# Performance work log

Hardware: AMD Instinct MI355X
Metric: run time of the kernel (lower is better)

Reference implementation:

```python
import jax, jax.numpy as jnp
import numpy as np

N_HEADS = 16  # matches init_kwargs

def setup_inputs() -> dict:
    key = jax.random.key(0)
    kq, kk, kv = jax.random.split(key, 3)
    B, L, S, D = 4, 2048, 2048, 1024
    queries = jax.random.normal(kq, (B, L, D), dtype=jnp.float32)
    keys = jax.random.normal(kk, (B, S, D), dtype=jnp.float32)
    values = jax.random.normal(kv, (B, S, D), dtype=jnp.float32)
    # TriangularCausalMask: True above the diagonal (positions to mask)
    causal = jnp.triu(jnp.ones((L, S), dtype=bool), k=1)
    attn_mask = jnp.broadcast_to(causal[None, None], (B, 1, L, S))
    return {"queries": queries, "keys": keys, "values": values, "attn_mask": attn_mask}

def reference(queries, keys, values, attn_mask):
    B, L, _ = queries.shape
    S = keys.shape[1]
    H = N_HEADS
    q = queries.reshape(B, L, H, -1)   # (B,L,H,E)
    k = keys.reshape(B, S, H, -1)      # (B,S,H,E)
    v = values.reshape(B, S, H, -1)    # (B,S,H,E)
    scale = 1.0 / jnp.sqrt(jnp.asarray(q.shape[-1], dtype=q.dtype))
    scores = jnp.einsum('blhe,bshe->bhls', q, k)          # (B,H,L,S)
    scores = jnp.where(attn_mask, -jnp.inf, scores)        # masked_fill_
    A = jax.nn.softmax(scale * scores, axis=-1)            # dropout is identity (p=0 / eval)
    V = jnp.einsum('bhls,bshd->blhd', A, v)                # (B,L,H,E)
    return V.reshape(B, L, -1)
```

## Files before the change

kernel.cpp:

```cpp
#include <hip/hip_runtime.h>
#include <hip/hip_bf16.h>

typedef __attribute__((ext_vector_type(8))) short short8;
typedef __attribute__((ext_vector_type(4))) short short4v;
typedef __attribute__((ext_vector_type(4))) float floatx4;

constexpr int B = 4, L = 2048, H = 16, E = 64, D = 1024;
constexpr int STR = 72;
constexpr float SCL_LOG2E = 0.125f * 1.4426950408889634f;

__device__ __forceinline__ short bf16_bits(float x) {
    __hip_bfloat16 b = __float2bfloat16(x);
    return *(const short*)&b;
}

__device__ __forceinline__ short8 packq8(float4 a, float4 c, float scl) {
    short8 r;
    r[0] = bf16_bits(a.x * scl); r[1] = bf16_bits(a.y * scl);
    r[2] = bf16_bits(a.z * scl); r[3] = bf16_bits(a.w * scl);
    r[4] = bf16_bits(c.x * scl); r[5] = bf16_bits(c.y * scl);
    r[6] = bf16_bits(c.z * scl); r[7] = bf16_bits(c.w * scl);
    return r;
}

__device__ __forceinline__ void load_lds16(const short* g, short* l) {
    __builtin_amdgcn_global_load_lds(
        (const __attribute__((address_space(1))) unsigned int*)g,
        (__attribute__((address_space(3))) unsigned int*)l, 16, 0, 0);
}

__global__ __launch_bounds__(256)
void prep_kv(const float* __restrict__ K, const float* __restrict__ V,
             short* __restrict__ Kb, short* __restrict__ Vt)
{
    __shared__ __align__(16) short vt[64 * STR];
    const int tid = threadIdx.x;
    const int bh = blockIdx.x >> 5, kt = blockIdx.x & 31;
    const int b = bh >> 4, h = bh & 15;

    const float* Kp = K + ((size_t)(b * L + kt * 64)) * D + h * E;
    const float* Vp = V + ((size_t)(b * L + kt * 64)) * D + h * E;
    short* Kop = Kb + ((size_t)(bh * 32 + kt)) * 4096;
    short* Vop = Vt + ((size_t)(bh * 32 + kt)) * 4096;

    #pragma unroll
    for (int it = 0; it < 2; ++it) {
        int f = it * 256 + tid;
        int nt = f >> 7, hh = (f >> 6) & 1, qd = (f >> 4) & 3, cc = f & 15;
        int s = nt * 16 + cc, d0 = hh * 32 + qd * 8;
        const float* p = Kp + (size_t)s * D + d0;
        float4 x = *(const float4*)p;
        float4 y = *(const float4*)(p + 4);
        union { short sh[8]; uint4 u; } pk;
        pk.sh[0] = bf16_bits(x.x); pk.sh[1] = bf16_bits(x.y);
        pk.sh[2] = bf16_bits(x.z); pk.sh[3] = bf16_bits(x.w);
        pk.sh[4] = bf16_bits(y.x); pk.sh[5] = bf16_bits(y.y);
        pk.sh[6] = bf16_bits(y.z); pk.sh[7] = bf16_bits(y.w);
        *(uint4*)(Kop + (size_t)f * 8) = pk.u;
    }

    #pragma unroll
    for (int p = 0; p < 4; ++p) {
        int idx = p * 256 + tid;
        int s = idx >> 4, c4 = (idx & 15) * 4;
        float4 g = *(const float4*)(Vp + (size_t)s * D + c4);
        vt[(c4 + 0) * STR + s] = bf16_bits(g.x);
        vt[(c4 + 1) * STR + s] = bf16_bits(g.y);
        vt[(c4 + 2) * STR + s] = bf16_bits(g.z);
        vt[(c4 + 3) * STR + s] = bf16_bits(g.w);
    }
    __syncthreads();

    #pragma unroll
    for (int it = 0; it < 2; ++it) {
        int f16 = it * 256 + tid;
        int f8 = f16 * 2;
        int st = f8 >> 8, dt = (f8 >> 6) & 3, qd = (f8 >> 4) & 3;
        int cA = f8 & 15;
        int dA = dt * 16 + cA, dB = dA + 1;
        int s0 = st * 16 + qd * 4;
        uint2 a = *(const uint2*)&vt[dA * STR + s0];
        uint2 c = *(const uint2*)&vt[dB * STR + s0];
        uint4 u; u.x = a.x; u.y = a.y; u.z = c.x; u.w = c.y;
        *(uint4*)(Vop + (size_t)f16 * 8) = u;
    }
}

__device__ __forceinline__ void step_single(
    const short* __restrict__ kc, const short* __restrict__ vc,
    short8 qf0, short8 qf1, int mrow, int s_base, int cnt, bool diag,
    floatx4 (&o)[4], float& lsum, int lane)
{
    short4v pa[4];
    #pragma unroll
    for (int nt = 0; nt < 4; ++nt) {
        if (nt < cnt) {
            short8 kb0 = *(const short8*)&kc[nt * 1024 + lane * 8];
            short8 kb1 = *(const short8*)&kc[nt * 1024 + 512 + lane * 8];
            floatx4 acc = (floatx4){0.f, 0.f, 0.f, 0.f};
            acc = __builtin_amdgcn_mfma_f32_16x16x32_bf16(kb0, qf0, acc, 0, 0, 0);
            acc = __builtin_amdgcn_mfma_f32_16x16x32_bf16(kb1, qf1, acc, 0, 0, 0);
            if (diag && nt == cnt - 1) {
                const int s0 = s_base + nt * 16;
                #pragma unroll
                for (int r = 0; r < 4; ++r)
                    if (s0 + r > mrow) acc[r] = -__builtin_inff();
            }
            #pragma unroll
            for (int r = 0; r < 4; ++r) {
                float p = __builtin_amdgcn_exp2f(acc[r]);
                lsum += p;
                pa[nt][r] = bf16_bits(p);
            }
        }
    }
    #pragma unroll
    for (int st = 0; st < 4; ++st) {
        if (st < cnt) {
            #pragma unroll
            for (int dt = 0; dt < 4; ++dt) {
                short4v vb = *(const short4v*)&vc[(st * 4 + dt) * 256 + lane * 4];
                o[dt] = __builtin_amdgcn_mfma_f32_16x16x16bf16_1k(pa[st], vb, o[dt], 0, 0, 0);
            }
        }
    }
}

__device__ __forceinline__ void step_merged(
    const short* __restrict__ kc, const short* __restrict__ vc,
    short8 qfA0, short8 qfA1, short8 qfB0, short8 qfB1,
    int mrowB, int s_base, int cntB, bool diagB,
    floatx4 (&oA)[4], floatx4 (&oB)[4], float& lA, float& lB, int lane)
{
    short4v paA[4], paB[4];
    #pragma unroll
    for (int nt = 0; nt < 4; ++nt) {
        short8 kb0 = *(const short8*)&kc[nt * 1024 + lane * 8];
        short8 kb1 = *(const short8*)&kc[nt * 1024 + 512 + lane * 8];
        floatx4 a = (floatx4){0.f, 0.f, 0.f, 0.f};
        a = __builtin_amdgcn_mfma_f32_16x16x32_bf16(kb0, qfA0, a, 0, 0, 0);
        a = __builtin_amdgcn_mfma_f32_16x16x32_bf16(kb1, qfA1, a, 0, 0, 0);
        #pragma unroll
        for (int r = 0; r < 4; ++r) {
            float p = __builtin_amdgcn_exp2f(a[r]);
            lA += p;
            paA[nt][r] = bf16_bits(p);
        }
        if (nt < cntB) {
            floatx4 bb = (floatx4){0.f, 0.f, 0.f, 0.f};
            bb = __builtin_amdgcn_mfma_f32_16x16x32_bf16(kb0, qfB0, bb, 0, 0, 0);
            bb = __builtin_amdgcn_mfma_f32_16x16x32_bf16(kb1, qfB1, bb, 0, 0, 0);
            if (diagB && nt == cntB - 1) {
                const int s0 = s_base + nt * 16;
                #pragma unroll
                for (int r = 0; r < 4; ++r)
                    if (s0 + r > mrowB) bb[r] = -__builtin_inff();
            }
            #pragma unroll
            for (int r = 0; r < 4; ++r) {
                float p = __builtin_amdgcn_exp2f(bb[r]);
                lB += p;
                paB[nt][r] = bf16_bits(p);
            }
        }
    }
    #pragma unroll
    for (int st = 0; st < 4; ++st) {
        #pragma unroll
        for (int dt = 0; dt < 4; ++dt) {
            short4v vb = *(const short4v*)&vc[(st * 4 + dt) * 256 + lane * 4];
            oA[dt] = __builtin_amdgcn_mfma_f32_16x16x16bf16_1k(paA[st], vb, oA[dt], 0, 0, 0);
            if (st < cntB)
                oB[dt] = __builtin_amdgcn_mfma_f32_16x16x16bf16_1k(paB[st], vb, oB[dt], 0, 0, 0);
        }
    }
}

__device__ __forceinline__ void store_frag(
    float lsum, const floatx4 (&o)[4], float* __restrict__ Op,
    int row_base, int c16, int quad)
{
    lsum += __shfl_xor(lsum, 16);
    lsum += __shfl_xor(lsum, 32);
    const int row0 = row_base + quad * 4;
    #pragma unroll
    for (int r = 0; r < 4; ++r) {
        const float inv = 1.f / __shfl(lsum, quad * 4 + r);
        #pragma unroll
        for (int dt = 0; dt < 4; ++dt)
            Op[(size_t)(row0 + r) * D + dt * 16 + c16] = o[dt][r] * inv;
    }
}

__global__ __launch_bounds__(256, 4)
void attn_fwd_p(const float* __restrict__ Q, const short* __restrict__ Kb,
                const short* __restrict__ Vt, float* __restrict__ O)
{
    __shared__ __align__(16) short k_s[2 * 4096];
    __shared__ __align__(16) short v_s[2 * 4096];

    const int tid  = threadIdx.x;
    const int wave = tid >> 6;
    const int lane = tid & 63;
    const int c16  = lane & 15;
    const int quad = lane >> 4;

    const int i  = (int)blockIdx.x;
    const int bh = ((i >> 7) << 3) | (i & 7);
    const int pp = (i >> 3) & 15;
    const int b  = bh >> 4;
    const int h  = bh & 15;

    const float* Qp  = Q  + ((size_t)b * L) * D + h * E;
    const short* Kbp = Kb + ((size_t)bh * 32) * 4096;
    const short* Vtp = Vt + ((size_t)bh * 32) * 4096;
    float*       Op  = O  + ((size_t)b * L) * D + h * E;

    const int qtA = 31 - pp, qtB = pp;
    const int nA  = qtA + 1;
    const int mA  = qtA * 64 + wave * 16;
    const int mB  = qtB * 64 + wave * 16;

    const float* qra = Qp + (size_t)(mA + c16) * D + quad * 8;
    short8 qfA0 = packq8(*(const float4*)(qra),      *(const float4*)(qra + 4),  SCL_LOG2E);
    short8 qfA1 = packq8(*(const float4*)(qra + 32), *(const float4*)(qra + 36), SCL_LOG2E);
    const float* qrb = Qp + (size_t)(mB + c16) * D + quad * 8;
    short8 qfB0 = packq8(*(const float4*)(qrb),      *(const float4*)(qrb + 4),  SCL_LOG2E);
    short8 qfB1 = packq8(*(const float4*)(qrb + 32), *(const float4*)(qrb + 36), SCL_LOG2E);

    #pragma unroll
    for (int it = 0; it < 2; ++it) {
        int c = it * 256 + tid;
        load_lds16(Kbp + (size_t)c * 8, k_s + c * 8);
        load_lds16(Vtp + (size_t)c * 8, v_s + c * 8);
    }

    floatx4 oA[4], oB[4];
    #pragma unroll
    for (int dt = 0; dt < 4; ++dt) {
        oA[dt] = (floatx4){0.f, 0.f, 0.f, 0.f};
        oB[dt] = (floatx4){0.f, 0.f, 0.f, 0.f};
    }
    float lA = 0.f, lB = 0.f;

    for (int t = 0; t < nA; ++t) {
        __syncthreads();
        const short* kc = k_s + (t & 1) * 4096;
        const short* vc = v_s + (t & 1) * 4096;

        if (t + 1 < nA) {
            const size_t nb = (size_t)(t + 1) * 4096;
            short* kn = k_s + ((t + 1) & 1) * 4096;
            short* vn = v_s + ((t + 1) & 1) * 4096;
            #pragma unroll
            for (int it = 0; it < 2; ++it) {
                int c = it * 256 + tid;
                load_lds16(Kbp + nb + (size_t)c * 8, kn + c * 8);
                load_lds16(Vtp + nb + (size_t)c * 8, vn + c * 8);
            }
        }

        __builtin_amdgcn_s_setprio(1);
        const int sb = t * 64 + quad * 4;
        if (t < qtB) {
            step_merged(kc, vc, qfA0, qfA1, qfB0, qfB1, 0, sb, 4, false,
                        oA, oB, lA, lB, lane);
        } else if (t == qtB) {
            step_merged(kc, vc, qfA0, qfA1, qfB0, qfB1, mB + c16, sb, wave + 1, true,
                        oA, oB, lA, lB, lane);
        } else if (t < qtA) {
            step_single(kc, vc, qfA0, qfA1, 0, sb, 4, false, oA, lA, lane);
        } else {
            step_single(kc, vc, qfA0, qfA1, mA + c16, sb, wave + 1, true, oA, lA, lane);
        }
        __builtin_amdgcn_s_setprio(0);
    }

    store_frag(lA, oA, Op, mA, c16, quad);
    store_frag(lB, oB, Op, mB, c16, quad);
}

__global__ __launch_bounds__(256, 2)
void attn_fwd_fb(const float* __restrict__ Q, const float* __restrict__ K,
                 const float* __restrict__ V, float* __restrict__ O)
{
    constexpr int FSTR = 72;
    constexpr int FQT = 64;
    __shared__ __align__(16) short q_s[FQT * FSTR];
    __shared__ __align__(16) short k_s[64 * FSTR];
    __shared__ __align__(16) short vt_s[E * FSTR];
    __shared__ __align__(16) short p_s[4][16 * FSTR];

    const int tid  = threadIdx.x;
    const int wave = tid >> 6;
    const int lane = tid & 63;
    const int c16  = lane & 15;
    const int quad = lane >> 4;

    const int nqt = L / FQT;
    const int qt  = (nqt - 1) - (int)(blockIdx.x % nqt);
    const int bh  = blockIdx.x / nqt;
    const int b   = bh >> 4;
    const int h   = bh & 15;
    const int q_base = qt * FQT;

    const float* Qp = Q + ((size_t)b * L) * D + h * E;
    const float* Kp = K + ((size_t)b * L) * D + h * E;
    const float* Vp = V + ((size_t)b * L) * D + h * E;
    float*       Op = O + ((size_t)b * L) * D + h * E;

    #pragma unroll
    for (int p = 0; p < 4; ++p) {
        int idx = p * 256 + tid;
        int r = idx >> 4, c4 = (idx & 15) * 4;
        float4 f = *(const float4*)(Qp + (size_t)(q_base + r) * D + c4);
        union { short s[4]; uint2 u; } pk;
        pk.s[0] = bf16_bits(f.x); pk.s[1] = bf16_bits(f.y);
        pk.s[2] = bf16_bits(f.z); pk.s[3] = bf16_bits(f.w);
        *(uint2*)&q_s[r * FSTR + c4] = pk.u;
    }
    __syncthreads();

    short8 qf0 = *(const short8*)&q_s[(wave * 16 + c16) * FSTR + quad * 8];
    short8 qf1 = *(const short8*)&q_s[(wave * 16 + c16) * FSTR + 32 + quad * 8];

    floatx4 o_acc[4];
    #pragma unroll
    for (int nt = 0; nt < 4; ++nt) o_acc[nt] = (floatx4){0.f, 0.f, 0.f, 0.f};
    float m_run[4], l_run[4];
    #pragma unroll
    for (int r = 0; r < 4; ++r) { m_run[r] = -__builtin_inff(); l_run[r] = 0.f; }

    for (int t = 0; t <= qt; ++t) {
        const int k_base = t * 64;
        __syncthreads();
        #pragma unroll
        for (int p = 0; p < 4; ++p) {
            int idx = p * 256 + tid;
            int r = idx >> 4, c4 = (idx & 15) * 4;
            float4 f = *(const float4*)(Kp + (size_t)(k_base + r) * D + c4);
            union { short s[4]; uint2 u; } pk;
            pk.s[0] = bf16_bits(f.x); pk.s[1] = bf16_bits(f.y);
            pk.s[2] = bf16_bits(f.z); pk.s[3] = bf16_bits(f.w);
            *(uint2*)&k_s[r * FSTR + c4] = pk.u;
        }
        #pragma unroll
        for (int p = 0; p < 4; ++p) {
            int s  = lane;
            int dg = p * 4 + wave;
            float4 f = *(const float4*)(Vp + (size_t)(k_base + s) * D + dg * 4);
            vt_s[(dg * 4 + 0) * FSTR + s] = bf16_bits(f.x);
            vt_s[(dg * 4 + 1) * FSTR + s] = bf16_bits(f.y);
            vt_s[(dg * 4 + 2) * FSTR + s] = bf16_bits(f.z);
            vt_s[(dg * 4 + 3) * FSTR + s] = bf16_bits(f.w);
        }
        __syncthreads();

        floatx4 sc[4];
        #pragma unroll
        for (int nt = 0; nt < 4; ++nt) {
            floatx4 acc = (floatx4){0.f, 0.f, 0.f, 0.f};
            short8 b0 = *(const short8*)&k_s[(nt * 16 + c16) * FSTR + quad * 8];
            short8 b1 = *(const short8*)&k_s[(nt * 16 + c16) * FSTR + 32 + quad * 8];
            acc = __builtin_amdgcn_mfma_f32_16x16x32_bf16(qf0, b0, acc, 0, 0, 0);
            acc = __builtin_amdgcn_mfma_f32_16x16x32_bf16(qf1, b1, acc, 0, 0, 0);
            sc[nt] = acc;
        }

        const int q_row0 = q_base + wave * 16 + quad * 4;
        #pragma unroll
        for (int nt = 0; nt < 4; ++nt) {
            const int k_col = k_base + nt * 16 + c16;
            #pragma unroll
            for (int r = 0; r < 4; ++r) {
                float s = sc[nt][r] * SCL_LOG2E;
                sc[nt][r] = (k_col <= q_row0 + r) ? s : -__builtin_inff();
            }
        }

        float alpha[4];
        #pragma unroll
        for (int r = 0; r < 4; ++r) {
            float mx = fmaxf(fmaxf(sc[0][r], sc[1][r]), fmaxf(sc[2][r], sc[3][r]));
            mx = fmaxf(mx, __shfl_xor(mx, 1));
            mx = fmaxf(mx, __shfl_xor(mx, 2));
            mx = fmaxf(mx, __shfl_xor(mx, 4));
            mx = fmaxf(mx, __shfl_xor(mx, 8));
            const float m_new = fmaxf(m_run[r], mx);
            alpha[r] = exp2f(m_run[r] - m_new);
            m_run[r] = m_new;
        }
        float psum[4] = {0.f, 0.f, 0.f, 0.f};
        #pragma unroll
        for (int nt = 0; nt < 4; ++nt) {
            #pragma unroll
            for (int r = 0; r < 4; ++r) {
                float p = exp2f(sc[nt][r] - m_run[r]);
                sc[nt][r] = p;
                psum[r] += p;
            }
        }
        #pragma unroll
        for (int r = 0; r < 4; ++r) {
            float s = psum[r];
            s += __shfl_xor(s, 1);
            s += __shfl_xor(s, 2);
            s += __shfl_xor(s, 4);
            s += __shfl_xor(s, 8);
            l_run[r] = l_run[r] * alpha[r] + s;
            #pragma unroll
            for (int nt = 0; nt < 4; ++nt) o_acc[nt][r] *= alpha[r];
        }

        short* pw = &p_s[wave][0];
        #pragma unroll
        for (int nt = 0; nt < 4; ++nt) {
            #pragma unroll
            for (int r = 0; r < 4; ++r)
                pw[(quad * 4 + r) * FSTR + nt * 16 + c16] = bf16_bits(sc[nt][r]);
        }
        __syncthreads();

        #pragma unroll
        for (int kc = 0; kc < 2; ++kc) {
            short8 pa = *(const short8*)&pw[c16 * FSTR + kc * 32 + quad * 8];
            #pragma unroll
            for (int nt = 0; nt < 4; ++nt) {
                short8 vb = *(const short8*)&vt_s[(nt * 16 + c16) * FSTR + kc * 32 + quad * 8];
                o_acc[nt] = __builtin_amdgcn_mfma_f32_16x16x32_bf16(pa, vb, o_acc[nt], 0, 0, 0);
            }
        }
    }

    const int q_row0 = q_base + wave * 16 + quad * 4;
    #pragma unroll
    for (int r = 0; r < 4; ++r) {
        const float inv_l = 1.f / l_run[r];
        #pragma unroll
        for (int nt = 0; nt < 4; ++nt)
            Op[(size_t)(q_row0 + r) * D + nt * 16 + c16] = o_acc[nt][r] * inv_l;
    }
}

extern "C" void kernel_launch(void* const* d_in, const int* in_sizes, int n_in,
                              void* d_out, int out_size, void* d_ws, size_t ws_size,
                              hipStream_t stream)
{
    const float* Q = (const float*)d_in[0];
    const float* K = (const float*)d_in[1];
    const float* V = (const float*)d_in[2];
    float* O = (float*)d_out;

    const size_t elems = (size_t)B * H * L * E;
    const size_t need  = 2 * elems * sizeof(short);

    if (ws_size >= need) {
        short* Kb = (short*)d_ws;
        short* Vt = Kb + elems;
        prep_kv<<<dim3(B * H * 32), dim3(256), 0, stream>>>(K, V, Kb, Vt);
        attn_fwd_p<<<dim3(B * H * 16), dim3(256), 0, stream>>>(Q, Kb, Vt, O);
    } else {
        attn_fwd_fb<<<dim3(B * H * (L / 64)), dim3(256), 0, stream>>>(Q, K, V, O);
    }
}
```

Before: 242.5 us.

## Replace paired short/long query tiles with contiguous 128-row tiles per block

Each block now handles one contiguous 128-row query tile, with each wave owning 32 consecutive rows (two 16-row fragments), instead of pairing a long and a short 64-row tile for load balance. Both fragments share every K/V tile loaded into LDS. Block work now varies with the tile index, and waves whose diagonal tile comes earlier sit idle for the final iterations. The goal is to reduce the per-step branching and to simplify the causal handling to a single diagonal step per wave.

```diff
diff --git a/kernel.cpp b/kernel.cpp
--- a/kernel.cpp
+++ b/kernel.cpp
@@ -86,92 +86,98 @@
     }
 }
 
-__device__ __forceinline__ void step_single(
+__device__ __forceinline__ void step_full(
     const short* __restrict__ kc, const short* __restrict__ vc,
-    short8 qf0, short8 qf1, int mrow, int s_base, int cnt, bool diag,
-    floatx4 (&o)[4], float& lsum, int lane)
-{
-    short4v pa[4];
-    #pragma unroll
-    for (int nt = 0; nt < 4; ++nt) {
-        if (nt < cnt) {
-            short8 kb0 = *(const short8*)&kc[nt * 1024 + lane * 8];
-            short8 kb1 = *(const short8*)&kc[nt * 1024 + 512 + lane * 8];
-            floatx4 acc = (floatx4){0.f, 0.f, 0.f, 0.f};
-            acc = __builtin_amdgcn_mfma_f32_16x16x32_bf16(kb0, qf0, acc, 0, 0, 0);
-            acc = __builtin_amdgcn_mfma_f32_16x16x32_bf16(kb1, qf1, acc, 0, 0, 0);
-            if (diag && nt == cnt - 1) {
-                const int s0 = s_base + nt * 16;
-                #pragma unroll
-                for (int r = 0; r < 4; ++r)
-                    if (s0 + r > mrow) acc[r] = -__builtin_inff();
-            }
-            #pragma unroll
-            for (int r = 0; r < 4; ++r) {
-                float p = __builtin_amdgcn_exp2f(acc[r]);
-                lsum += p;
-                pa[nt][r] = bf16_bits(p);
-            }
-        }
-    }
-    #pragma unroll
-    for (int st = 0; st < 4; ++st) {
-        if (st < cnt) {
-            #pragma unroll
-            for (int dt = 0; dt < 4; ++dt) {
-                short4v vb = *(const short4v*)&vc[(st * 4 + dt) * 256 + lane * 4];
-                o[dt] = __builtin_amdgcn_mfma_f32_16x16x16bf16_1k(pa[st], vb, o[dt], 0, 0, 0);
-            }
-        }
-    }
-}
-
-__device__ __forceinline__ void step_merged(
-    const short* __restrict__ kc, const short* __restrict__ vc,
-    short8 qfA0, short8 qfA1, short8 qfB0, short8 qfB1,
-    int mrowB, int s_base, int cntB, bool diagB,
-    floatx4 (&oA)[4], floatx4 (&oB)[4], float& lA, float& lB, int lane)
-{
-    short4v paA[4], paB[4];
+    short8 q00, short8 q01, short8 q10, short8 q11,
+    floatx4 (&o0)[4], floatx4 (&o1)[4], float& l0, float& l1, int lane)
+{
+    short4v p0[4], p1[4];
     #pragma unroll
     for (int nt = 0; nt < 4; ++nt) {
         short8 kb0 = *(const short8*)&kc[nt * 1024 + lane * 8];
         short8 kb1 = *(const short8*)&kc[nt * 1024 + 512 + lane * 8];
-        floatx4 a = (floatx4){0.f, 0.f, 0.f, 0.f};
-        a = __builtin_amdgcn_mfma_f32_16x16x32_bf16(kb0, qfA0, a, 0, 0, 0);
-        a = __builtin_amdgcn_mfma_f32_16x16x32_bf16(kb1, qfA1, a, 0, 0, 0);
+        floatx4 a0 = (floatx4){0.f, 0.f, 0.f, 0.f};
+        a0 = __builtin_amdgcn_mfma_f32_16x16x32_bf16(kb0, q00, a0, 0, 0, 0);
+        a0 = __builtin_amdgcn_mfma_f32_16x16x32_bf16(kb1, q01, a0, 0, 0, 0);
+        floatx4 a1 = (floatx4){0.f, 0.f, 0.f, 0.f};
+        a1 = __builtin_amdgcn_mfma_f32_16x16x32_bf16(kb0, q10, a1, 0, 0, 0);
+        a1 = __builtin_amdgcn_mfma_f32_16x16x32_bf16(kb1, q11, a1, 0, 0, 0);
         #pragma unroll
         for (int r = 0; r < 4; ++r) {
-            float p = __builtin_amdgcn_exp2f(a[r]);
-            lA += p;
-            paA[nt][r] = bf16_bits(p);
-        }
-        if (nt < cntB) {
-            floatx4 bb = (floatx4){0.f, 0.f, 0.f, 0.f};
-            bb = __builtin_amdgcn_mfma_f32_16x16x32_bf16(kb0, qfB0, bb, 0, 0, 0);
-            bb = __builtin_amdgcn_mfma_f32_16x16x32_bf16(kb1, qfB1, bb, 0, 0, 0);
-            if (diagB && nt == cntB - 1) {
-                const int s0 = s_base + nt * 16;
+            float pa = __builtin_amdgcn_exp2f(a0[r]);
+            float pb = __builtin_amdgcn_exp2f(a1[r]);
+            l0 += pa; l1 += pb;
+            p0[nt][r] = bf16_bits(pa);
+            p1[nt][r] = bf16_bits(pb);
+        }
+    }
+    #pragma unroll
+    for (int st = 0; st < 4; ++st) {
+        #pragma unroll
+        for (int dt = 0; dt < 4; ++dt) {
+            short4v vb = *(const short4v*)&vc[(st * 4 + dt) * 256 + lane * 4];
+            o0[dt] = __builtin_amdgcn_mfma_f32_16x16x16bf16_1k(p0[st], vb, o0[dt], 0, 0, 0);
+            o1[dt] = __builtin_amdgcn_mfma_f32_16x16x16bf16_1k(p1[st], vb, o1[dt], 0, 0, 0);
+        }
+    }
+}
+
+__device__ __forceinline__ void step_diag(
+    const short* __restrict__ kc, const short* __restrict__ vc,
+    short8 q00, short8 q01, short8 q10, short8 q11,
+    int cnt0, int mrow0, int s_base,
+    floatx4 (&o0)[4], floatx4 (&o1)[4], float& l0, float& l1, int lane)
+{
+    const int cnt1 = cnt0 + 1;
+    short4v p0[4], p1[4];
+    #pragma unroll
+    for (int nt = 0; nt < 4; ++nt) {
+        if (nt < cnt1) {
+            short8 kb0 = *(const short8*)&kc[nt * 1024 + lane * 8];
+            short8 kb1 = *(const short8*)&kc[nt * 1024 + 512 + lane * 8];
+            const int s0 = s_base + nt * 16;
+            floatx4 a1 = (floatx4){0.f, 0.f, 0.f, 0.f};
+            a1 = __builtin_amdgcn_mfma_f32_16x16x32_bf16(kb0, q10, a1, 0, 0, 0);
+            a1 = __builtin_amdgcn_mfma_f32_16x16x32_bf16(kb1, q11, a1, 0, 0, 0);
+            if (nt == cnt0) {
                 #pragma unroll
                 for (int r = 0; r < 4; ++r)
-                    if (s0 + r > mrowB) bb[r] = -__builtin_inff();
+                    if (s0 + r > mrow0 + 16) a1[r] = -__builtin_inff();
             }
             #pragma unroll
             for (int r = 0; r < 4; ++r) {
-                float p = __builtin_amdgcn_exp2f(bb[r]);
-                lB += p;
-                paB[nt][r] = bf16_bits(p);
+                float pb = __builtin_amdgcn_exp2f(a1[r]);
+                l1 += pb;
+                p1[nt][r] = bf16_bits(pb);
+            }
+            if (nt < cnt0) {
+                floatx4 a0 = (floatx4){0.f, 0.f, 0.f, 0.f};
+                a0 = __builtin_amdgcn_mfma_f32_16x16x32_bf16(kb0, q00, a0, 0, 0, 0);
+                a0 = __builtin_amdgcn_mfma_f32_16x16x32_bf16(kb1, q01, a0, 0, 0, 0);
+                if (nt == cnt0 - 1) {
+                    #pragma unroll
+                    for (int r = 0; r < 4; ++r)
+                        if (s0 + r > mrow0) a0[r] = -__builtin_inff();
+                }
+                #pragma unroll
+                for (int r = 0; r < 4; ++r) {
+                    float pa = __builtin_amdgcn_exp2f(a0[r]);
+                    l0 += pa;
+                    p0[nt][r] = bf16_bits(pa);
+                }
             }
         }
     }
     #pragma unroll
     for (int st = 0; st < 4; ++st) {
-        #pragma unroll
-        for (int dt = 0; dt < 4; ++dt) {
-            short4v vb = *(const short4v*)&vc[(st * 4 + dt) * 256 + lane * 4];
-            oA[dt] = __builtin_amdgcn_mfma_f32_16x16x16bf16_1k(paA[st], vb, oA[dt], 0, 0, 0);
-            if (st < cntB)
-                oB[dt] = __builtin_amdgcn_mfma_f32_16x16x16bf16_1k(paB[st], vb, oB[dt], 0, 0, 0);
+        if (st < cnt1) {
+            #pragma unroll
+            for (int dt = 0; dt < 4; ++dt) {
+                short4v vb = *(const short4v*)&vc[(st * 4 + dt) * 256 + lane * 4];
+                o1[dt] = __builtin_amdgcn_mfma_f32_16x16x16bf16_1k(p1[st], vb, o1[dt], 0, 0, 0);
+                if (st < cnt0)
+                    o0[dt] = __builtin_amdgcn_mfma_f32_16x16x16bf16_1k(p0[st], vb, o0[dt], 0, 0, 0);
+            }
         }
     }
 }
@@ -207,7 +213,7 @@
 
     const int i  = (int)blockIdx.x;
     const int bh = ((i >> 7) << 3) | (i & 7);
-    const int pp = (i >> 3) & 15;
+    const int qt = 15 - ((i >> 3) & 15);
     const int b  = bh >> 4;
     const int h  = bh & 15;
 
@@ -216,17 +222,17 @@
     const short* Vtp = Vt + ((size_t)bh * 32) * 4096;
     float*       Op  = O  + ((size_t)b * L) * D + h * E;
 
-    const int qtA = 31 - pp, qtB = pp;
-    const int nA  = qtA + 1;
-    const int mA  = qtA * 64 + wave * 16;
-    const int mB  = qtB * 64 + wave * 16;
-
-    const float* qra = Qp + (size_t)(mA + c16) * D + quad * 8;
-    short8 qfA0 = packq8(*(const float4*)(qra),      *(const float4*)(qra + 4),  SCL_LOG2E);
-    short8 qfA1 = packq8(*(const float4*)(qra + 32), *(const float4*)(qra + 36), SCL_LOG2E);
-    const float* qrb = Qp + (size_t)(mB + c16) * D + quad * 8;
-    short8 qfB0 = packq8(*(const float4*)(qrb),      *(const float4*)(qrb + 4),  SCL_LOG2E);
-    short8 qfB1 = packq8(*(const float4*)(qrb + 32), *(const float4*)(qrb + 36), SCL_LOG2E);
+    const int n_tiles = 2 * qt + 2;
+    const int m0  = qt * 128 + wave * 32;
+    const int t_d = 2 * qt + (wave >> 1);
+    const int cnt0 = (wave & 1) ? 3 : 1;
+
+    const float* qr0 = Qp + (size_t)(m0 + c16) * D + quad * 8;
+    short8 q00 = packq8(*(const float4*)(qr0),      *(const float4*)(qr0 + 4),  SCL_LOG2E);
+    short8 q01 = packq8(*(const float4*)(qr0 + 32), *(const float4*)(qr0 + 36), SCL_LOG2E);
+    const float* qr1 = qr0 + (size_t)16 * D;
+    short8 q10 = packq8(*(const float4*)(qr1),      *(const float4*)(qr1 + 4),  SCL_LOG2E);
+    short8 q11 = packq8(*(const float4*)(qr1 + 32), *(const float4*)(qr1 + 36), SCL_LOG2E);
 
     #pragma unroll
     for (int it = 0; it < 2; ++it) {
@@ -235,20 +241,20 @@
         load_lds16(Vtp + (size_t)c * 8, v_s + c * 8);
     }
 
-    floatx4 oA[4], oB[4];
+    floatx4 o0[4], o1[4];
     #pragma unroll
     for (int dt = 0; dt < 4; ++dt) {
-        oA[dt] = (floatx4){0.f, 0.f, 0.f, 0.f};
-        oB[dt] = (floatx4){0.f, 0.f, 0.f, 0.f};
-    }
-    float lA = 0.f, lB = 0.f;
-
-    for (int t = 0; t < nA; ++t) {
+        o0[dt] = (floatx4){0.f, 0.f, 0.f, 0.f};
+        o1[dt] = (floatx4){0.f, 0.f, 0.f, 0.f};
+    }
+    float l0 = 0.f, l1 = 0.f;
+
+    for (int t = 0; t < n_tiles; ++t) {
         __syncthreads();
         const short* kc = k_s + (t & 1) * 4096;
         const short* vc = v_s + (t & 1) * 4096;
 
-        if (t + 1 < nA) {
+        if (t + 1 < n_tiles) {
             const size_t nb = (size_t)(t + 1) * 4096;
             short* kn = k_s + ((t + 1) & 1) * 4096;
             short* vn = v_s + ((t + 1) & 1) * 4096;
@@ -261,23 +267,17 @@
         }
 
         __builtin_amdgcn_s_setprio(1);
-        const int sb = t * 64 + quad * 4;
-        if (t < qtB) {
-            step_merged(kc, vc, qfA0, qfA1, qfB0, qfB1, 0, sb, 4, false,
-                        oA, oB, lA, lB, lane);
-        } else if (t == qtB) {
-            step_merged(kc, vc, qfA0, qfA1, qfB0, qfB1, mB + c16, sb, wave + 1, true,
-                        oA, oB, lA, lB, lane);
-        } else if (t < qtA) {
-            step_single(kc, vc, qfA0, qfA1, 0, sb, 4, false, oA, lA, lane);
-        } else {
-            step_single(kc, vc, qfA0, qfA1, mA + c16, sb, wave + 1, true, oA, lA, lane);
+        if (t < t_d) {
+            step_full(kc, vc, q00, q01, q10, q11, o0, o1, l0, l1, lane);
+        } else if (t == t_d) {
+            step_diag(kc, vc, q00, q01, q10, q11, cnt0, m0 + c16,
+                      t * 64 + quad * 4, o0, o1, l0, l1, lane);
         }
         __builtin_amdgcn_s_setprio(0);
     }
 
-    store_frag(lA, oA, Op, mA, c16, quad);
-    store_frag(lB, oB, Op, mB, c16, quad);
+    store_frag(l0, o0, Op, m0, c16, quad);
+    store_frag(l1, o1, Op, m0 + 16, c16, quad);
 }
 
 __global__ __launch_bounds__(256, 2)
```

After: 238.0 us. No clear change (-1.8%).
